# Performance work log

Hardware: AMD Instinct MI355X
Metric: run time of the kernel (lower is better)

Reference implementation:

```python
import jax, jax.numpy as jnp
import numpy as np

NMS_SIGMA = 2.0
MASK_THRESH = 0.5
N = 500
H = W = 256
NUM_CLS = 80


def setup_inputs() -> dict:
    key = jax.random.key(0)
    k1, k2, k3 = jax.random.split(key, 3)
    mask_preds = jax.random.uniform(k1, (N, H, W), dtype=jnp.float32)
    cate_scores = jax.random.uniform(k2, (N,), dtype=jnp.float32)
    cate_labels = jax.random.randint(k3, (N,), 0, NUM_CLS, dtype=jnp.int32)
    return {"mask_preds": mask_preds, "cate_scores": cate_scores, "cate_labels": cate_labels}


def reference(mask_preds, cate_scores, cate_labels):
    n = mask_preds.shape[0]
    # binarize masks (SOLOv2 inference: seg_masks = seg_preds > mask_thresh)
    seg_masks = (mask_preds > MASK_THRESH).astype(mask_preds.dtype)  # [N,H,W]
    sum_masks = seg_masks.sum(axis=(1, 2))                           # [N]
    # mask scoring: average soft score inside the binary mask
    seg_scores = (mask_preds * seg_masks).sum(axis=(1, 2)) / jnp.maximum(sum_masks, 1.0)
    scores = cate_scores * seg_scores                                # [N]
    # sort descending by score (matrix-NMS assumes sorted order)
    order = jnp.argsort(-scores)
    scores = scores[order]
    labels = cate_labels[order]
    flat = seg_masks[order].reshape(n, -1)                           # [N,HW]
    sums = sum_masks[order]
    # pairwise mask IoU, upper-triangular (j suppressed by i<j)
    inter = flat @ flat.T                                            # [N,N]
    union = sums[:, None] + sums[None, :] - inter
    iou = jnp.triu(inter / jnp.maximum(union, 1.0), k=1)
    label_match = jnp.triu((labels[:, None] == labels[None, :]).astype(iou.dtype), k=1)
    decay_iou = iou * label_match                                    # [N,N]
    # gaussian matrix-NMS decay
    compensate_iou = decay_iou.max(axis=0)                           # [N]
    decay_matrix = jnp.exp(-NMS_SIGMA * (decay_iou ** 2 - compensate_iou[:, None] ** 2))
    coeff = decay_matrix.min(axis=0)                                 # [N]
    updated_scores = scores * coeff
    return updated_scores
```

## Files before the change

kernel.cpp:

```cpp
#include <hip/hip_runtime.h>
#include <cstdint>

typedef unsigned long long u64;

#define THRESH 0.5f
#define SIGMA 2.0f
#define TPB 64
#define NSPLIT 16
#define CST 66
#define MAXN 512

__device__ __forceinline__ bool better(float sa, int a, float sb, int b) {
    return (sa > sb) || (sa == sb && a < b);
}

__global__ __launch_bounds__(256) void k_pack(
    const float* __restrict__ preds, u64* __restrict__ packed,
    double* __restrict__ pssum, int* __restrict__ pcnt, int HW)
{
    const int task = blockIdx.x;
    const int i = task >> 2, sub = task & 3;
    const int seg = HW >> 2;
    const float* src = preds + (size_t)i * HW + (size_t)sub * seg;
    u64* dst = packed + (size_t)i * (HW >> 6) + (size_t)sub * (seg >> 6);
    const int tid = threadIdx.x;
    const int wave = tid >> 6, lane = tid & 63;
    double ssum = 0.0;
    int cnt = 0;
    const int iters = seg >> 12;
    for (int k = 0; k < iters; ++k) {
        const int base = (k << 12) + (wave << 10) + (lane << 2);
        const float4 v0 = *reinterpret_cast<const float4*>(src + base);
        const float4 v1 = *reinterpret_cast<const float4*>(src + base + 256);
        const float4 v2 = *reinterpret_cast<const float4*>(src + base + 512);
        const float4 v3 = *reinterpret_cast<const float4*>(src + base + 768);
        #pragma unroll
        for (int q = 0; q < 4; ++q) {
            const float4 v = (q == 0) ? v0 : (q == 1) ? v1 : (q == 2) ? v2 : v3;
            const bool b0 = v.x > THRESH, b1 = v.y > THRESH, b2 = v.z > THRESH, b3 = v.w > THRESH;
            const u64 m0 = __ballot(b0);
            const u64 m1 = __ballot(b1);
            const u64 m2 = __ballot(b2);
            const u64 m3 = __ballot(b3);
            if (lane < 4) {
                const u64 m = (lane == 0) ? m0 : (lane == 1) ? m1 : (lane == 2) ? m2 : m3;
                dst[(k << 6) + (wave << 4) + (q << 2) + lane] = m;
            }
            cnt += (int)b0 + (int)b1 + (int)b2 + (int)b3;
            ssum += (b0 ? (double)v.x : 0.0) + (b1 ? (double)v.y : 0.0)
                  + (b2 ? (double)v.z : 0.0) + (b3 ? (double)v.w : 0.0);
        }
    }
    for (int off = 32; off > 0; off >>= 1) {
        ssum += __shfl_down(ssum, off);
        cnt  += __shfl_down(cnt, off);
    }
    __shared__ double ls[4];
    __shared__ int lc[4];
    if (lane == 0) { ls[wave] = ssum; lc[wave] = cnt; }
    __syncthreads();
    if (tid == 0) {
        pssum[task] = ls[0] + ls[1] + ls[2] + ls[3];
        pcnt[task]  = lc[0] + lc[1] + lc[2] + lc[3];
    }
}

__global__ __launch_bounds__(256) void k_inter(
    const u64* __restrict__ packed, unsigned* __restrict__ part,
    int N, int WORDS, int NT)
{
    __shared__ __align__(16) u64 sm[2 * TPB][CST];
    int b = blockIdx.x;
    int ti = 0, rowlen = NT;
    while (b >= rowlen) { b -= rowlen; ++ti; --rowlen; }
    const int tj = ti + b;
    const int kwords = WORDS / NSPLIT;
    const int kbase = blockIdx.y * kwords;

    const int tid = threadIdx.x;
    const int a = tid >> 4, bb = tid & 15;

    const int half = kwords >> 1;
    for (int idx = tid; idx < 2 * TPB * half; idx += 256) {
        const int ml = idx / half;
        const int w = (idx - ml * half) << 1;
        const int g = (ml < TPB) ? (ti * TPB + ml) : (tj * TPB + (ml - TPB));
        u64 x0 = 0, x1 = 0;
        if (g < N) {
            const u64* p = packed + (size_t)g * WORDS + kbase + w;
            x0 = p[0];
            x1 = p[1];
        }
        sm[ml][w] = x0;
        sm[ml][w + 1] = x1;
    }
    __syncthreads();

    unsigned acc[4][4] = {};
    #pragma unroll 4
    for (int w = 0; w < kwords; w += 2) {
        u64 pi0[4], pi1[4], pj0[4], pj1[4];
        #pragma unroll
        for (int t = 0; t < 4; ++t) {
            const ulonglong2 q = *reinterpret_cast<const ulonglong2*>(&sm[4 * a + t][w]);
            pi0[t] = q.x; pi1[t] = q.y;
        }
        #pragma unroll
        for (int s = 0; s < 4; ++s) {
            const ulonglong2 q = *reinterpret_cast<const ulonglong2*>(&sm[TPB + bb + 16 * s][w]);
            pj0[s] = q.x; pj1[s] = q.y;
        }
        #pragma unroll
        for (int t = 0; t < 4; ++t)
            #pragma unroll
            for (int s = 0; s < 4; ++s)
                acc[t][s] += (unsigned)__popcll(pi0[t] & pj0[s])
                           + (unsigned)__popcll(pi1[t] & pj1[s]);
    }
    #pragma unroll
    for (int t = 0; t < 4; ++t)
        #pragma unroll
        for (int s = 0; s < 4; ++s) {
            const int gi = ti * TPB + 4 * a + t;
            const int gj = tj * TPB + bb + 16 * s;
            if (gj < N && gi < gj)
                part[((size_t)gi * N + gj) * NSPLIT + blockIdx.y] = acc[t][s];
        }
}

__device__ __forceinline__ unsigned fold16(const unsigned* __restrict__ p) {
    const uint4* q = reinterpret_cast<const uint4*>(p);
    unsigned s = 0;
    #pragma unroll
    for (int k = 0; k < 4; ++k) {
        const uint4 v = q[k];
        s += v.x + v.y + v.z + v.w;
    }
    return s;
}

__device__ __forceinline__ void finalize_scores(
    const double* __restrict__ pssum, const int* __restrict__ pcnt,
    const float* __restrict__ cate, const int* __restrict__ labels,
    float* s_score, float* s_sum, int* s_label, int N, int tid)
{
    for (int idx = tid; idx < N; idx += 256) {
        const double S = ((pssum[4*idx] + pssum[4*idx+1]) + pssum[4*idx+2]) + pssum[4*idx+3];
        const int C = ((pcnt[4*idx] + pcnt[4*idx+1]) + pcnt[4*idx+2]) + pcnt[4*idx+3];
        s_score[idx] = cate[idx] * (float)(S / (double)(C > 1 ? C : 1));
        s_sum[idx] = (float)C;
        s_label[idx] = labels[idx];
    }
    __syncthreads();
}

__global__ __launch_bounds__(256) void k_comp(
    const unsigned* __restrict__ part,
    const double* __restrict__ pssum, const int* __restrict__ pcnt,
    const float* __restrict__ cate, const int* __restrict__ labels,
    float* __restrict__ comp, int N)
{
    __shared__ float s_score[MAXN];
    __shared__ float s_sum[MAXN];
    __shared__ int s_label[MAXN];
    const int tid = threadIdx.x;
    finalize_scores(pssum, pcnt, cate, labels, s_score, s_sum, s_label, N, tid);

    const int bI = blockIdx.x;
    const float sb = s_score[bI], sub = s_sum[bI];
    const int lb = s_label[bI];
    float m = 0.0f;
    for (int a = tid; a < N; a += 256) {
        if (a == bI || s_label[a] != lb) continue;
        if (!better(s_score[a], a, sb, bI)) continue;
        const int lo = a < bI ? a : bI, hi = a < bI ? bI : a;
        const float inter = (float)fold16(part + ((size_t)lo * N + hi) * NSPLIT);
        const float un = s_sum[a] + sub - inter;
        m = fmaxf(m, inter / fmaxf(un, 1.0f));
    }
    for (int off = 32; off > 0; off >>= 1) m = fmaxf(m, __shfl_down(m, off));
    __shared__ float lm[4];
    const int wave = tid >> 6, lane = tid & 63;
    if (lane == 0) lm[wave] = m;
    __syncthreads();
    if (tid == 0) comp[bI] = fmaxf(fmaxf(lm[0], lm[1]), fmaxf(lm[2], lm[3]));
}

__global__ __launch_bounds__(256) void k_final(
    const unsigned* __restrict__ part,
    const double* __restrict__ pssum, const int* __restrict__ pcnt,
    const float* __restrict__ cate, const int* __restrict__ labels,
    const float* __restrict__ comp, float* __restrict__ out, int N)
{
    __shared__ float s_score[MAXN];
    __shared__ float s_sum[MAXN];
    __shared__ int s_label[MAXN];
    const int tid = threadIdx.x;
    finalize_scores(pssum, pcnt, cate, labels, s_score, s_sum, s_label, N, tid);

    const int bI = blockIdx.x;
    const float sb = s_score[bI], sub = s_sum[bI];
    const int lb = s_label[bI];
    float m = -3.0e38f;
    int r = 0;
    for (int a = tid; a < N; a += 256) {
        const bool bet = (a != bI) && better(s_score[a], a, sb, bI);
        r += (int)bet;
        float d = 0.0f;
        if (bet && s_label[a] == lb) {
            const int lo = a < bI ? a : bI, hi = a < bI ? bI : a;
            const float inter = (float)fold16(part + ((size_t)lo * N + hi) * NSPLIT);
            const float un = s_sum[a] + sub - inter;
            d = inter / fmaxf(un, 1.0f);
        }
        const float ca = comp[a];
        m = fmaxf(m, d * d - ca * ca);
    }
    for (int off = 32; off > 0; off >>= 1) {
        m = fmaxf(m, __shfl_down(m, off));
        r += __shfl_down(r, off);
    }
    __shared__ float lm[4];
    __shared__ int lr[4];
    const int wave = tid >> 6, lane = tid & 63;
    if (lane == 0) { lm[wave] = m; lr[wave] = r; }
    __syncthreads();
    if (tid == 0) {
        const float mm = fmaxf(fmaxf(lm[0], lm[1]), fmaxf(lm[2], lm[3]));
        const int rank = lr[0] + lr[1] + lr[2] + lr[3];
        out[rank] = sb * expf(-SIGMA * mm);
    }
}

extern "C" void kernel_launch(void* const* d_in, const int* in_sizes, int n_in,
                              void* d_out, int out_size, void* d_ws, size_t ws_size,
                              hipStream_t stream)
{
    const float* preds  = (const float*)d_in[0];
    const float* cate   = (const float*)d_in[1];
    const int*   labels = (const int*)d_in[2];
    float* out = (float*)d_out;

    const int N = in_sizes[1];
    const int HW = in_sizes[0] / N;
    const int WORDS = HW >> 6;

    char* ws = (char*)d_ws;
    size_t off = 0;
    auto take = [&](size_t bytes) -> void* {
        void* p = ws + off;
        off = (off + bytes + 255) & ~(size_t)255;
        return p;
    };
    u64*      packed = (u64*)     take((size_t)N * WORDS * sizeof(u64));
    double*   pssum  = (double*)  take((size_t)N * 4 * sizeof(double));
    int*      pcnt   = (int*)     take((size_t)N * 4 * sizeof(int));
    float*    comp   = (float*)   take((size_t)N * sizeof(float));
    unsigned* part   = (unsigned*)take((size_t)N * N * NSPLIT * sizeof(unsigned));
    (void)ws_size; (void)n_in; (void)out_size;

    k_pack<<<N * 4, 256, 0, stream>>>(preds, packed, pssum, pcnt, HW);

    const int NT = (N + TPB - 1) / TPB;
    dim3 grid(NT * (NT + 1) / 2, NSPLIT);
    k_inter<<<grid, 256, 0, stream>>>(packed, part, N, WORDS, NT);

    k_comp<<<N, 256, 0, stream>>>(part, pssum, pcnt, cate, labels, comp, N);

    k_final<<<N, 256, 0, stream>>>(part, pssum, pcnt, cate, labels, comp, out, N);
}
```

Measured before the change: 244.1 us.

## Fuse comp and final NMS stages into last-block tail of intersection kernel

The intersection kernel now accumulates each pair's count into a single N×N buffer with atomicAdd, instead of writing 16 split partials per pair. That buffer and the completion counter are zeroed inside the pack kernel. The last block to finish, found with an atomic ticket, computes scores, sort keys, ranks, compensation IoU and decayed scores in shared memory. It caches up to 16 same-label predecessors per box to avoid a second full scan. This removes two kernel launches and the 16-partial write and reduce traffic, at the cost of atomics and a serial single-block tail over all N boxes.

```diff
diff --git a/kernel.cpp b/kernel.cpp
--- a/kernel.cpp
+++ b/kernel.cpp
@@ -9,14 +9,31 @@
 #define NSPLIT 16
 #define CST 66
 #define MAXN 512
-
-__device__ __forceinline__ bool better(float sa, int a, float sb, int b) {
-    return (sa > sb) || (sa == sb && a < b);
-}
+#define CAP 16
+
+struct TailShared {
+    u64 key[MAXN];
+    float score[MAXN];
+    float sum[MAXN];
+    int label[MAXN];
+    float comp[MAXN];
+    unsigned short cnt[MAXN];
+    unsigned short rank[MAXN];
+    unsigned short alist[MAXN][CAP];
+    float dlist[MAXN][CAP];
+    int isLast;
+};
+
+union InterShared {
+    u64 sm[2 * TPB][CST];
+    TailShared t;
+};
 
 __global__ __launch_bounds__(256) void k_pack(
     const float* __restrict__ preds, u64* __restrict__ packed,
-    double* __restrict__ pssum, int* __restrict__ pcnt, int HW)
+    double* __restrict__ pssum, int* __restrict__ pcnt,
+    unsigned* __restrict__ interFull, unsigned* __restrict__ doneCnt,
+    int N, int HW)
 {
     const int task = blockIdx.x;
     const int i = task >> 2, sub = task & 3;
@@ -25,6 +42,17 @@
     u64* dst = packed + (size_t)i * (HW >> 6) + (size_t)sub * (seg >> 6);
     const int tid = threadIdx.x;
     const int wave = tid >> 6, lane = tid & 63;
+
+    {
+        const size_t NN = (size_t)N * N;
+        const size_t zbase = (size_t)task * 128;
+        for (int z = tid; z < 128; z += 256) {
+            const size_t idx = zbase + (size_t)z;
+            if (idx < NN) interFull[idx] = 0u;
+        }
+        if (task == 0 && tid == 0) *doneCnt = 0u;
+    }
+
     double ssum = 0.0;
     int cnt = 0;
     const int iters = seg >> 12;
@@ -66,169 +94,161 @@
 }
 
 __global__ __launch_bounds__(256) void k_inter(
-    const u64* __restrict__ packed, unsigned* __restrict__ part,
-    int N, int WORDS, int NT)
+    const u64* __restrict__ packed, unsigned* __restrict__ interFull,
+    unsigned* __restrict__ doneCnt,
+    const double* __restrict__ pssum, const int* __restrict__ pcnt,
+    const float* __restrict__ cate, const int* __restrict__ labels,
+    float* __restrict__ out, int N, int WORDS, int NT)
 {
-    __shared__ __align__(16) u64 sm[2 * TPB][CST];
-    int b = blockIdx.x;
-    int ti = 0, rowlen = NT;
-    while (b >= rowlen) { b -= rowlen; ++ti; --rowlen; }
-    const int tj = ti + b;
-    const int kwords = WORDS / NSPLIT;
-    const int kbase = blockIdx.y * kwords;
-
+    __shared__ InterShared sh;
+    __shared__ float gred[4];
     const int tid = threadIdx.x;
-    const int a = tid >> 4, bb = tid & 15;
-
-    const int half = kwords >> 1;
-    for (int idx = tid; idx < 2 * TPB * half; idx += 256) {
-        const int ml = idx / half;
-        const int w = (idx - ml * half) << 1;
-        const int g = (ml < TPB) ? (ti * TPB + ml) : (tj * TPB + (ml - TPB));
-        u64 x0 = 0, x1 = 0;
-        if (g < N) {
-            const u64* p = packed + (size_t)g * WORDS + kbase + w;
-            x0 = p[0];
-            x1 = p[1];
-        }
-        sm[ml][w] = x0;
-        sm[ml][w + 1] = x1;
-    }
-    __syncthreads();
-
-    unsigned acc[4][4] = {};
-    #pragma unroll 4
-    for (int w = 0; w < kwords; w += 2) {
-        u64 pi0[4], pi1[4], pj0[4], pj1[4];
-        #pragma unroll
-        for (int t = 0; t < 4; ++t) {
-            const ulonglong2 q = *reinterpret_cast<const ulonglong2*>(&sm[4 * a + t][w]);
-            pi0[t] = q.x; pi1[t] = q.y;
-        }
-        #pragma unroll
-        for (int s = 0; s < 4; ++s) {
-            const ulonglong2 q = *reinterpret_cast<const ulonglong2*>(&sm[TPB + bb + 16 * s][w]);
-            pj0[s] = q.x; pj1[s] = q.y;
+    const int wave = tid >> 6, lane = tid & 63;
+
+    {
+        int b = blockIdx.x;
+        int ti = 0, rowlen = NT;
+        while (b >= rowlen) { b -= rowlen; ++ti; --rowlen; }
+        const int tj = ti + b;
+        const int kwords = WORDS / NSPLIT;
+        const int kbase = blockIdx.y * kwords;
+        const int a = tid >> 4, bb = tid & 15;
+
+        const int half = kwords >> 1;
+        for (int idx = tid; idx < 2 * TPB * half; idx += 256) {
+            const int ml = idx / half;
+            const int w = (idx - ml * half) << 1;
+            const int g = (ml < TPB) ? (ti * TPB + ml) : (tj * TPB + (ml - TPB));
+            u64 x0 = 0, x1 = 0;
+            if (g < N) {
+                const u64* p = packed + (size_t)g * WORDS + kbase + w;
+                x0 = p[0];
+                x1 = p[1];
+            }
+            sh.sm[ml][w] = x0;
+            sh.sm[ml][w + 1] = x1;
+        }
+        __syncthreads();
+
+        unsigned acc[4][4] = {};
+        #pragma unroll 4
+        for (int w = 0; w < kwords; w += 2) {
+            u64 pi0[4], pi1[4], pj0[4], pj1[4];
+            #pragma unroll
+            for (int t = 0; t < 4; ++t) {
+                const ulonglong2 q = *reinterpret_cast<const ulonglong2*>(&sh.sm[4 * a + t][w]);
+                pi0[t] = q.x; pi1[t] = q.y;
+            }
+            #pragma unroll
+            for (int s = 0; s < 4; ++s) {
+                const ulonglong2 q = *reinterpret_cast<const ulonglong2*>(&sh.sm[TPB + bb + 16 * s][w]);
+                pj0[s] = q.x; pj1[s] = q.y;
+            }
+            #pragma unroll
+            for (int t = 0; t < 4; ++t)
+                #pragma unroll
+                for (int s = 0; s < 4; ++s)
+                    acc[t][s] += (unsigned)__popcll(pi0[t] & pj0[s])
+                               + (unsigned)__popcll(pi1[t] & pj1[s]);
         }
         #pragma unroll
         for (int t = 0; t < 4; ++t)
             #pragma unroll
-            for (int s = 0; s < 4; ++s)
-                acc[t][s] += (unsigned)__popcll(pi0[t] & pj0[s])
-                           + (unsigned)__popcll(pi1[t] & pj1[s]);
-    }
-    #pragma unroll
-    for (int t = 0; t < 4; ++t)
-        #pragma unroll
-        for (int s = 0; s < 4; ++s) {
-            const int gi = ti * TPB + 4 * a + t;
-            const int gj = tj * TPB + bb + 16 * s;
-            if (gj < N && gi < gj)
-                part[((size_t)gi * N + gj) * NSPLIT + blockIdx.y] = acc[t][s];
-        }
-}
-
-__device__ __forceinline__ unsigned fold16(const unsigned* __restrict__ p) {
-    const uint4* q = reinterpret_cast<const uint4*>(p);
-    unsigned s = 0;
-    #pragma unroll
-    for (int k = 0; k < 4; ++k) {
-        const uint4 v = q[k];
-        s += v.x + v.y + v.z + v.w;
-    }
-    return s;
-}
-
-__device__ __forceinline__ void finalize_scores(
-    const double* __restrict__ pssum, const int* __restrict__ pcnt,
-    const float* __restrict__ cate, const int* __restrict__ labels,
-    float* s_score, float* s_sum, int* s_label, int N, int tid)
-{
-    for (int idx = tid; idx < N; idx += 256) {
-        const double S = ((pssum[4*idx] + pssum[4*idx+1]) + pssum[4*idx+2]) + pssum[4*idx+3];
-        const int C = ((pcnt[4*idx] + pcnt[4*idx+1]) + pcnt[4*idx+2]) + pcnt[4*idx+3];
-        s_score[idx] = cate[idx] * (float)(S / (double)(C > 1 ? C : 1));
-        s_sum[idx] = (float)C;
-        s_label[idx] = labels[idx];
-    }
-    __syncthreads();
-}
-
-__global__ __launch_bounds__(256) void k_comp(
-    const unsigned* __restrict__ part,
-    const double* __restrict__ pssum, const int* __restrict__ pcnt,
-    const float* __restrict__ cate, const int* __restrict__ labels,
-    float* __restrict__ comp, int N)
-{
-    __shared__ float s_score[MAXN];
-    __shared__ float s_sum[MAXN];
-    __shared__ int s_label[MAXN];
-    const int tid = threadIdx.x;
-    finalize_scores(pssum, pcnt, cate, labels, s_score, s_sum, s_label, N, tid);
-
-    const int bI = blockIdx.x;
-    const float sb = s_score[bI], sub = s_sum[bI];
-    const int lb = s_label[bI];
-    float m = 0.0f;
-    for (int a = tid; a < N; a += 256) {
-        if (a == bI || s_label[a] != lb) continue;
-        if (!better(s_score[a], a, sb, bI)) continue;
-        const int lo = a < bI ? a : bI, hi = a < bI ? bI : a;
-        const float inter = (float)fold16(part + ((size_t)lo * N + hi) * NSPLIT);
-        const float un = s_sum[a] + sub - inter;
-        m = fmaxf(m, inter / fmaxf(un, 1.0f));
-    }
-    for (int off = 32; off > 0; off >>= 1) m = fmaxf(m, __shfl_down(m, off));
-    __shared__ float lm[4];
-    const int wave = tid >> 6, lane = tid & 63;
-    if (lane == 0) lm[wave] = m;
-    __syncthreads();
-    if (tid == 0) comp[bI] = fmaxf(fmaxf(lm[0], lm[1]), fmaxf(lm[2], lm[3]));
-}
-
-__global__ __launch_bounds__(256) void k_final(
-    const unsigned* __restrict__ part,
-    const double* __restrict__ pssum, const int* __restrict__ pcnt,
-    const float* __restrict__ cate, const int* __restrict__ labels,
-    const float* __restrict__ comp, float* __restrict__ out, int N)
-{
-    __shared__ float s_score[MAXN];
-    __shared__ float s_sum[MAXN];
-    __shared__ int s_label[MAXN];
-    const int tid = threadIdx.x;
-    finalize_scores(pssum, pcnt, cate, labels, s_score, s_sum, s_label, N, tid);
-
-    const int bI = blockIdx.x;
-    const float sb = s_score[bI], sub = s_sum[bI];
-    const int lb = s_label[bI];
-    float m = -3.0e38f;
-    int r = 0;
-    for (int a = tid; a < N; a += 256) {
-        const bool bet = (a != bI) && better(s_score[a], a, sb, bI);
-        r += (int)bet;
-        float d = 0.0f;
-        if (bet && s_label[a] == lb) {
-            const int lo = a < bI ? a : bI, hi = a < bI ? bI : a;
-            const float inter = (float)fold16(part + ((size_t)lo * N + hi) * NSPLIT);
-            const float un = s_sum[a] + sub - inter;
-            d = inter / fmaxf(un, 1.0f);
-        }
-        const float ca = comp[a];
-        m = fmaxf(m, d * d - ca * ca);
-    }
-    for (int off = 32; off > 0; off >>= 1) {
-        m = fmaxf(m, __shfl_down(m, off));
-        r += __shfl_down(r, off);
-    }
-    __shared__ float lm[4];
-    __shared__ int lr[4];
-    const int wave = tid >> 6, lane = tid & 63;
-    if (lane == 0) { lm[wave] = m; lr[wave] = r; }
+            for (int s = 0; s < 4; ++s) {
+                const int gi = ti * TPB + 4 * a + t;
+                const int gj = tj * TPB + bb + 16 * s;
+                if (gj < N && gi < gj)
+                    atomicAdd(&interFull[(size_t)gi * N + gj], acc[t][s]);
+            }
+    }
+
     __syncthreads();
     if (tid == 0) {
-        const float mm = fmaxf(fmaxf(lm[0], lm[1]), fmaxf(lm[2], lm[3]));
-        const int rank = lr[0] + lr[1] + lr[2] + lr[3];
-        out[rank] = sb * expf(-SIGMA * mm);
+        __threadfence();
+        const unsigned total = gridDim.x * gridDim.y;
+        const unsigned prev = atomicAdd(doneCnt, 1u);
+        sh.t.isLast = (prev == total - 1u) ? 1 : 0;
+    }
+    __syncthreads();
+    if (!sh.t.isLast) return;
+    __threadfence();
+
+    for (int b = tid; b < N; b += 256) {
+        const double S = ((pssum[4*b] + pssum[4*b+1]) + pssum[4*b+2]) + pssum[4*b+3];
+        const int C = ((pcnt[4*b] + pcnt[4*b+1]) + pcnt[4*b+2]) + pcnt[4*b+3];
+        const float sc = cate[b] * (float)(S / (double)(C > 1 ? C : 1));
+        sh.t.score[b] = sc;
+        sh.t.sum[b] = (float)C;
+        sh.t.label[b] = labels[b];
+        sh.t.key[b] = ((u64)__float_as_uint(sc) << 32) | (u64)(0xFFFFFFFFu - (unsigned)b);
+    }
+    __syncthreads();
+
+    for (int b = tid; b < N; b += 256) {
+        const u64 kb = sh.t.key[b];
+        const int lb = sh.t.label[b];
+        const float sub = sh.t.sum[b];
+        float cmax = 0.0f;
+        int r = 0, c = 0;
+        for (int a2 = 0; a2 < N; ++a2) {
+            if (sh.t.key[a2] > kb) {
+                ++r;
+                if (sh.t.label[a2] == lb) {
+                    const int lo = a2 < b ? a2 : b, hi = a2 < b ? b : a2;
+                    const unsigned iv = __hip_atomic_load(
+                        &interFull[(size_t)lo * N + hi],
+                        __ATOMIC_RELAXED, __HIP_MEMORY_SCOPE_AGENT);
+                    const float inter = (float)iv;
+                    const float un = sh.t.sum[a2] + sub - inter;
+                    const float d = inter / fmaxf(un, 1.0f);
+                    cmax = fmaxf(cmax, d);
+                    if (c < CAP) { sh.t.alist[b][c] = (unsigned short)a2; sh.t.dlist[b][c] = d; }
+                    ++c;
+                }
+            }
+        }
+        sh.t.comp[b] = cmax;
+        sh.t.rank[b] = (unsigned short)r;
+        sh.t.cnt[b] = (unsigned short)c;
+    }
+    __syncthreads();
+
+    float gm = 3.0e38f;
+    for (int b = tid; b < N; b += 256) gm = fminf(gm, sh.t.comp[b]);
+    for (int off = 32; off > 0; off >>= 1) gm = fminf(gm, __shfl_down(gm, off));
+    if (lane == 0) gred[wave] = gm;
+    __syncthreads();
+    const float gmin = fminf(fminf(gred[0], gred[1]), fminf(gred[2], gred[3]));
+
+    for (int b = tid; b < N; b += 256) {
+        float m = -(gmin * gmin);
+        const int c = sh.t.cnt[b];
+        if (c <= CAP) {
+            for (int k2 = 0; k2 < c; ++k2) {
+                const int a2 = sh.t.alist[b][k2];
+                const float d = sh.t.dlist[b][k2];
+                const float ca = sh.t.comp[a2];
+                m = fmaxf(m, d * d - ca * ca);
+            }
+        } else {
+            const u64 kb = sh.t.key[b];
+            const int lb = sh.t.label[b];
+            const float sub = sh.t.sum[b];
+            for (int a2 = 0; a2 < N; ++a2) {
+                if (sh.t.key[a2] > kb && sh.t.label[a2] == lb) {
+                    const int lo = a2 < b ? a2 : b, hi = a2 < b ? b : a2;
+                    const unsigned iv = __hip_atomic_load(
+                        &interFull[(size_t)lo * N + hi],
+                        __ATOMIC_RELAXED, __HIP_MEMORY_SCOPE_AGENT);
+                    const float inter = (float)iv;
+                    const float un = sh.t.sum[a2] + sub - inter;
+                    const float d = inter / fmaxf(un, 1.0f);
+                    const float ca = sh.t.comp[a2];
+                    m = fmaxf(m, d * d - ca * ca);
+                }
+            }
+        }
+        out[sh.t.rank[b]] = sh.t.score[b] * expf(-SIGMA * m);
     }
 }
 
@@ -252,20 +272,19 @@
         off = (off + bytes + 255) & ~(size_t)255;
         return p;
     };
-    u64*      packed = (u64*)     take((size_t)N * WORDS * sizeof(u64));
-    double*   pssum  = (double*)  take((size_t)N * 4 * sizeof(double));
-    int*      pcnt   = (int*)     take((size_t)N * 4 * sizeof(int));
-    float*    comp   = (float*)   take((size_t)N * sizeof(float));
-    unsigned* part   = (unsigned*)take((size_t)N * N * NSPLIT * sizeof(unsigned));
+    u64*      packed   = (u64*)     take((size_t)N * WORDS * sizeof(u64));
+    double*   pssum    = (double*)  take((size_t)N * 4 * sizeof(double));
+    int*      pcnt     = (int*)     take((size_t)N * 4 * sizeof(int));
+    unsigned* interFull= (unsigned*)take((size_t)N * N * sizeof(unsigned));
+    unsigned* doneCnt  = (unsigned*)take(sizeof(unsigned));
     (void)ws_size; (void)n_in; (void)out_size;
 
-    k_pack<<<N * 4, 256, 0, stream>>>(preds, packed, pssum, pcnt, HW);
+    k_pack<<<N * 4, 256, 0, stream>>>(preds, packed, pssum, pcnt,
+                                      interFull, doneCnt, N, HW);
 
     const int NT = (N + TPB - 1) / TPB;
     dim3 grid(NT * (NT + 1) / 2, NSPLIT);
-    k_inter<<<grid, 256, 0, stream>>>(packed, part, N, WORDS, NT);
-
-    k_comp<<<N, 256, 0, stream>>>(part, pssum, pcnt, cate, labels, comp, N);
-
-    k_final<<<N, 256, 0, stream>>>(part, pssum, pcnt, cate, labels, comp, out, N);
+    k_inter<<<grid, 256, 0, stream>>>(packed, interFull, doneCnt,
+                                      pssum, pcnt, cate, labels,
+                                      out, N, WORDS, NT);
 }
```

Result: slower. 458.0 us (+87.7%).
